# Performance work log

Hardware: AMD Instinct MI355X
Metric: run time of the kernel (lower is better)

## Reference

```python
import jax, jax.numpy as jnp
import numpy as np
import math

N_TOTAL = 262144
C = 128
B = 512
LMAX = 512  # max segment length (static for jit)


def setup_inputs() -> dict:
    key = jax.random.key(0)
    ks = jax.random.split(key, 8)
    Q_feature = jax.random.normal(ks[0], (N_TOTAL, C), dtype=jnp.float32)
    K_feature = jax.random.normal(ks[1], (N_TOTAL, C), dtype=jnp.float32)
    # cumulative offsets: equal segments of length LMAX (general code handles ragged)
    offset = (jnp.arange(1, B + 1, dtype=jnp.int64) * (N_TOTAL // B))
    s = 1.0 / math.sqrt(C)
    Wq = jax.random.normal(ks[2], (C, C), dtype=jnp.float32) * s
    Wk = jax.random.normal(ks[3], (C, C), dtype=jnp.float32) * s
    Wv = jax.random.normal(ks[4], (C, C), dtype=jnp.float32) * s
    bq = jnp.zeros((C,), dtype=jnp.float32)
    bk = jnp.zeros((C,), dtype=jnp.float32)
    bv = jnp.zeros((C,), dtype=jnp.float32)
    return {"Q_feature": Q_feature, "K_feature": K_feature,
            "Wq": Wq, "bq": bq, "Wk": Wk, "bk": bk, "Wv": Wv, "bv": bv,
            "offset": offset}


def reference(Q_feature, K_feature, Wq, bq, Wk, bk, Wv, bv, offset):
    N, Cdim = Q_feature.shape
    Q = Q_feature @ Wq.T + bq
    K = K_feature @ Wk.T + bk
    V = K_feature @ Wv.T + bv

    starts = jnp.concatenate([jnp.zeros((1,), offset.dtype), offset[:-1]])
    lengths = offset - starts                         # (B,)
    pos = jnp.arange(LMAX)                            # (LMAX,)
    idx = jnp.clip(starts[:, None] + pos[None, :], 0, N - 1)  # (B, LMAX)
    mask = pos[None, :] < lengths[:, None]            # (B, LMAX) valid tokens

    Qp = Q[idx]                                       # (B, LMAX, C)
    Kp = K[idx]
    Vp = V[idx]

    scale = 1.0 / math.sqrt(Cdim)
    scores = jnp.einsum('blc,bmc->blm', Qp, Kp) * scale     # (B, LMAX, LMAX)
    scores = jnp.where(mask[:, None, :], scores, jnp.float32(-1e30))
    attn = jax.nn.softmax(scores, axis=-1)
    outp = jnp.einsum('blm,bmc->blc', attn, Vp)             # (B, LMAX, C)
    outp = outp * mask[:, :, None]                          # zero padded rows

    # scatter padded segments back to flat (N, C); idx is an exact partition on valid rows
    out = jnp.zeros((N, Cdim), dtype=outp.dtype).at[idx].add(outp)
    return out
```

## Files before the change

kernel.cpp:

```cpp
#include <hip/hip_runtime.h>
#include <hip/hip_bf16.h>

#define CDIM 128
#define LMAXC 512
#define QBLK 128
#define KVBLK 64

#define QSCALE (0.08838834764831845f * 1.4426950408889634f)

typedef __attribute__((ext_vector_type(8))) short bf16x8;
typedef __attribute__((ext_vector_type(4))) short bf16x4;
typedef __attribute__((ext_vector_type(4))) float f32x4;

__device__ inline unsigned pk2(float lo, float hi) {
    unsigned r;
    asm("v_cvt_pk_bf16_f32 %0, %1, %2" : "=v"(r) : "v"(lo), "v"(hi));
    return r;
}

__device__ inline bf16x8 cvt8v(float4 a, float4 b) {
    union { bf16x8 v; unsigned u[4]; } t;
    t.u[0] = pk2(a.x, a.y); t.u[1] = pk2(a.z, a.w);
    t.u[2] = pk2(b.x, b.y); t.u[3] = pk2(b.z, b.w);
    return t.v;
}

__device__ inline void gload16(const void* g, void* l) {
    __builtin_amdgcn_global_load_lds(
        (const __attribute__((address_space(1))) unsigned*)g,
        (__attribute__((address_space(3))) unsigned*)l, 16, 0, 0);
}

__device__ inline void blk_barrier() {
    __builtin_amdgcn_sched_barrier(0);
    __builtin_amdgcn_s_barrier();
    __builtin_amdgcn_sched_barrier(0);
}

__device__ inline int pch(int q) { return ((q + (q >> 3)) & 7) << 4; }

__global__ void wcvt_kernel(const float* __restrict__ Wq,
                            const float* __restrict__ Wk,
                            const float* __restrict__ Wv,
                            short* __restrict__ Wbf)
{
    int t = blockIdx.x * 256 + threadIdx.x;
    int m = t / 2048;
    int e = (t % 2048) * 8;
    const float* W = (m == 0) ? Wq : (m == 1) ? Wk : Wv;
    float sc = (m == 0) ? QSCALE : 1.0f;
    float4 a = *reinterpret_cast<const float4*>(W + e);
    float4 b = *reinterpret_cast<const float4*>(W + e + 4);
    a.x *= sc; a.y *= sc; a.z *= sc; a.w *= sc;
    b.x *= sc; b.y *= sc; b.z *= sc; b.w *= sc;
    *reinterpret_cast<bf16x8*>(Wbf + m * 16384 + e) = cvt8v(a, b);
}

__global__ __launch_bounds__(256) void proj_kernel(
    const float* __restrict__ Qf, const float* __restrict__ Kf,
    const short* __restrict__ Wbf,
    const float* __restrict__ bq, const float* __restrict__ bk,
    const float* __restrict__ bv,
    short* __restrict__ Qp, short* __restrict__ Kp, short* __restrict__ Vt,
    int N)
{
    __shared__ __align__(16) char vt_lds[32768];

    const int tid   = threadIdx.x;
    const int lane  = tid & 63;
    const int wv    = tid >> 6;
    const int lrow  = lane & 15;
    const int lhalf = lane >> 4;
    const int row0  = blockIdx.x * 128;
    const bool isQ  = (blockIdx.y == 0);
    const float* X  = isQ ? Qf : Kf;

    bf16x8 xfr[2][4];
#pragma unroll
    for (int xt = 0; xt < 2; ++xt) {
        const float* xr = X + (size_t)(row0 + wv * 32 + xt * 16 + lrow) * CDIM;
#pragma unroll
        for (int ks = 0; ks < 4; ++ks) {
            const float4* s = reinterpret_cast<const float4*>(xr + ks * 32 + lhalf * 8);
            xfr[xt][ks] = cvt8v(s[0], s[1]);
        }
    }

    {
        const short* W    = isQ ? Wbf : Wbf + 16384;
        const float* bias = isQ ? bq : bk;
        const float  bsc  = isQ ? QSCALE : 1.0f;
        short* outp       = isQ ? Qp : Kp;

#pragma unroll
        for (int cf = 0; cf < 8; ++cf) {
            const short* wr = W + (cf * 16 + lrow) * CDIM;
            bf16x8 wfr[4];
#pragma unroll
            for (int ks = 0; ks < 4; ++ks)
                wfr[ks] = *reinterpret_cast<const bf16x8*>(wr + ks * 32 + lhalf * 8);
            float4 bv4 = *reinterpret_cast<const float4*>(bias + cf * 16 + lhalf * 4);
#pragma unroll
            for (int xt = 0; xt < 2; ++xt) {
                f32x4 acc = {0.f, 0.f, 0.f, 0.f};
#pragma unroll
                for (int ks = 0; ks < 4; ++ks)
                    acc = __builtin_amdgcn_mfma_f32_16x16x32_bf16(wfr[ks], xfr[xt][ks], acc, 0, 0, 0);
                union { bf16x4 v; unsigned u[2]; } pk;
                pk.u[0] = pk2(acc[0] + bv4.x * bsc, acc[1] + bv4.y * bsc);
                pk.u[1] = pk2(acc[2] + bv4.z * bsc, acc[3] + bv4.w * bsc);
                *reinterpret_cast<bf16x4*>(
                    outp + (size_t)(row0 + wv * 32 + xt * 16 + lrow) * CDIM
                         + cf * 16 + lhalf * 4) = pk.v;
            }
        }
    }

    if (!isQ) {
        const short* W = Wbf + 32768;
#pragma unroll
        for (int cf = 0; cf < 8; ++cf) {
            f32x4 acc0 = {0.f, 0.f, 0.f, 0.f};
            f32x4 acc1 = {0.f, 0.f, 0.f, 0.f};
            const short* wr = W + (cf * 16 + lrow) * CDIM;
#pragma unroll
            for (int ks = 0; ks < 4; ++ks) {
                bf16x8 bfr = *reinterpret_cast<const bf16x8*>(wr + ks * 32 + lhalf * 8);
                acc0 = __builtin_amdgcn_mfma_f32_16x16x32_bf16(xfr[0][ks], bfr, acc0, 0, 0, 0);
                acc1 = __builtin_amdgcn_mfma_f32_16x16x32_bf16(xfr[1][ks], bfr, acc1, 0, 0, 0);
            }
            const int col = cf * 16 + lrow;
            float bcol = bv[col];
            union { bf16x4 v; unsigned u[2]; } p0, p1;
            p0.u[0] = pk2(acc0[0] + bcol, acc0[1] + bcol);
            p0.u[1] = pk2(acc0[2] + bcol, acc0[3] + bcol);
            p1.u[0] = pk2(acc1[0] + bcol, acc1[1] + bcol);
            p1.u[1] = pk2(acc1[2] + bcol, acc1[3] + bcol);
            int base = col * 256 + wv * 64 + lhalf * 8;
            int sw   = (col & 7) << 4;
            *reinterpret_cast<bf16x4*>(vt_lds + ((base)      ^ sw)) = p0.v;
            *reinterpret_cast<bf16x4*>(vt_lds + ((base + 32) ^ sw)) = p1.v;
        }
        __syncthreads();
#pragma unroll
        for (int it = 0; it < 8; ++it) {
            int c   = it * 256 + tid;
            int col = c >> 4, rc = c & 15;
            int a   = (col * 256 + rc * 16) ^ ((col & 7) << 4);
            bf16x8 v = *reinterpret_cast<const bf16x8*>(vt_lds + a);
            *reinterpret_cast<bf16x8*>(Vt + (size_t)col * N + row0 + rc * 8) = v;
        }
    }
}

__global__ __launch_bounds__(256) void attn_kernel(
    const short* __restrict__ Qp, const short* __restrict__ Kp,
    const short* __restrict__ VtG, const int* __restrict__ offset,
    float* __restrict__ out, int Ntot)
{
    __shared__ __align__(16) char smem[81920];
    char* lds_p = smem + 65536;

    const int nq = LMAXC / QBLK;
    int flat = blockIdx.x, total = gridDim.x;
    int seg, qb;
    if ((total & (8 * nq - 1)) == 0) {
        int per = total >> 3;
        int xcd = flat & 7;
        int wi  = flat >> 3;
        int sl  = wi / nq;
        qb  = wi - sl * nq;
        seg = xcd * (per / nq) + sl;
    } else { seg = flat / nq; qb = flat - seg * nq; }

    const int start = (seg == 0) ? 0 : offset[seg - 1];
    int len = offset[seg] - start;
    if (len > LMAXC) len = LMAXC;
    const int q0 = qb * QBLK;
    if (q0 >= len) return;

    const int tid   = threadIdx.x;
    const int lane  = tid & 63;
    const int wv    = tid >> 6;
    const int lrow  = lane & 15;
    const int lhalf = lane >> 4;
    const int ntiles = (len + KVBLK - 1) / KVBLK;
    const int lm1 = len - 1;

    auto stage = [&](int kv0, int bb) {
        char* kb = smem + bb * 32768;
        char* vb = kb + 16384;
#pragma unroll
        for (int j = 0; j < 4; ++j) {
            int beta = j * 4096 + wv * 1024 + (lane << 4);
            int r  = beta >> 8;
            int gs = ((beta >> 4) & 15) ^ (r & 7);
            int rg = kv0 + r; if (rg > lm1) rg = lm1;
            gload16(Kp + (((size_t)(start + rg)) << 7) + (gs << 3),
                    kb + j * 4096 + wv * 1024);
            int d   = beta >> 7;
            int gs2 = ((beta >> 4) & 7) ^ (d & 7);
            long gk = (long)start + kv0 + (gs2 << 3);
            if (gk + 8 > Ntot) gk = Ntot - 8;
            gload16(VtG + (size_t)d * Ntot + gk,
                    vb + j * 4096 + wv * 1024);
        }
    };

    stage(0, 0);

    bf16x8 aq[2][4];
#pragma unroll
    for (int qt = 0; qt < 2; ++qt) {
        int qr = q0 + wv * 32 + qt * 16 + lrow;
        if (qr > lm1) qr = lm1;
        const short* qrow = Qp + (size_t)(start + qr) * CDIM;
#pragma unroll
        for (int ks = 0; ks < 4; ++ks)
            aq[qt][ks] = *reinterpret_cast<const bf16x8*>(qrow + ks * 32 + lhalf * 8);
    }

    f32x4 acc_o[2][8];
    float lsum[2] = {0.f, 0.f};
#pragma unroll
    for (int qt = 0; qt < 2; ++qt)
#pragma unroll
        for (int df = 0; df < 8; ++df) acc_o[qt][df] = (f32x4){0.f, 0.f, 0.f, 0.f};

    const int wbase = wv * 4096;

    for (int t = 0; t < ntiles; ++t) {
        const int kv0 = t * KVBLK;
        const int bb  = t & 1;
        if (t + 1 < ntiles) {
            stage(kv0 + KVBLK, bb ^ 1);
            asm volatile("s_waitcnt vmcnt(8)" ::: "memory");
        } else {
            asm volatile("s_waitcnt vmcnt(0)" ::: "memory");
        }
        blk_barrier();

        char* lds_k  = smem + bb * 32768;
        char* lds_vt = lds_k + 16384;
        const bool tail = (kv0 + KVBLK > len);

        f32x4 s0[4], s1[4];
        __builtin_amdgcn_s_setprio(1);
#pragma unroll
        for (int kf = 0; kf < 4; ++kf) {
            s0[kf] = (f32x4){0.f, 0.f, 0.f, 0.f};
            s1[kf] = (f32x4){0.f, 0.f, 0.f, 0.f};
            int key = kf * 16 + lrow;
#pragma unroll
            for (int ks = 0; ks < 4; ++ks) {
                int kbo = (key * 256 + (ks * 32 + lhalf * 8) * 2) ^ ((key & 7) << 4);
                bf16x8 kfr = *reinterpret_cast<const bf16x8*>(lds_k + kbo);
                s0[kf] = __builtin_amdgcn_mfma_f32_16x16x32_bf16(kfr, aq[0][ks], s0[kf], 0, 0, 0);
                s1[kf] = __builtin_amdgcn_mfma_f32_16x16x32_bf16(kfr, aq[1][ks], s1[kf], 0, 0, 0);
            }
        }
        __builtin_amdgcn_s_setprio(0);

        const int keyb0 = kv0 + lhalf * 4;
#pragma unroll
        for (int qt = 0; qt < 2; ++qt) {
            const int qlocal = qt * 16 + lrow;
            const int rowoff = wbase + qlocal * 128;
            const int swz = pch(qlocal);
#pragma unroll
            for (int kf = 0; kf < 4; ++kf) {
                f32x4 sv = qt ? s1[kf] : s0[kf];
                float p[4];
#pragma unroll
                for (int r = 0; r < 4; ++r) {
                    float pv = exp2f(sv[r]);
                    if (tail && (keyb0 + kf * 16 + r >= len)) pv = 0.f;
                    p[r] = pv;
                    lsum[qt] += pv;
                }
                unsigned long long w =
                    (unsigned long long)pk2(p[0], p[1]) |
                    ((unsigned long long)pk2(p[2], p[3]) << 32);
                *reinterpret_cast<unsigned long long*>(
                    lds_p + rowoff + ((kf * 32 + lhalf * 8) ^ swz)) = w;
            }
        }

        __builtin_amdgcn_s_setprio(1);
#pragma unroll
        for (int ks2 = 0; ks2 < 2; ++ks2) {
            bf16x8 ap0 = *reinterpret_cast<const bf16x8*>(
                lds_p + wbase + lrow * 128 + ((ks2 * 64 + lhalf * 16) ^ pch(lrow)));
            bf16x8 ap1 = *reinterpret_cast<const bf16x8*>(
                lds_p + wbase + (16 + lrow) * 128 + ((ks2 * 64 + lhalf * 16) ^ pch(16 + lrow)));
            int k0 = ks2 * 32 + lhalf * 8;
#pragma unroll
            for (int df = 0; df < 8; ++df) {
                int d = df * 16 + lrow;
                int vb2 = (d * 128 + k0 * 2) ^ ((d & 7) << 4);
                bf16x8 bvf = *reinterpret_cast<const bf16x8*>(lds_vt + vb2);
                acc_o[0][df] = __builtin_amdgcn_mfma_f32_16x16x32_bf16(ap0, bvf, acc_o[0][df], 0, 0, 0);
                acc_o[1][df] = __builtin_amdgcn_mfma_f32_16x16x32_bf16(ap1, bvf, acc_o[1][df], 0, 0, 0);
            }
        }
        __builtin_amdgcn_s_setprio(0);

        blk_barrier();
    }

#pragma unroll
    for (int qt = 0; qt < 2; ++qt) {
        float l = lsum[qt];
        l += __shfl_xor(l, 16);
        l += __shfl_xor(l, 32);
        float rinv[4];
#pragma unroll
        for (int r = 0; r < 4; ++r)
            rinv[r] = 1.0f / __shfl(l, lhalf * 4 + r);
#pragma unroll
        for (int df = 0; df < 8; ++df)
#pragma unroll
            for (int r = 0; r < 4; ++r) {
                int qg = q0 + wv * 32 + qt * 16 + lhalf * 4 + r;
                if (qg < len)
                    out[(size_t)(start + qg) * CDIM + df * 16 + lrow]
                        = acc_o[qt][df][r] * rinv[r];
            }
    }
}

extern "C" void kernel_launch(void* const* d_in, const int* in_sizes, int n_in,
                              void* d_out, int out_size, void* d_ws, size_t ws_size,
                              hipStream_t stream) {
    const float* Qf = (const float*)d_in[0];
    const float* Kf = (const float*)d_in[1];
    const float* Wq = (const float*)d_in[2];
    const float* bq = (const float*)d_in[3];
    const float* Wk = (const float*)d_in[4];
    const float* bk = (const float*)d_in[5];
    const float* Wv = (const float*)d_in[6];
    const float* bv_ = (const float*)d_in[7];
    const int* offset = (const int*)d_in[8];

    const int N = in_sizes[0] / CDIM;
    const int B = in_sizes[8];

    short* Qp = (short*)d_ws;
    short* Kp = Qp + (size_t)N * CDIM;
    short* Vt = Kp + (size_t)N * CDIM;
    float* out = (float*)d_out;

    size_t base_need = (size_t)3 * N * CDIM * 2;
    short* Wbf = (ws_size >= base_need + 3 * 16384 * 2)
               ? (Vt + (size_t)N * CDIM) : (short*)d_out;

    wcvt_kernel<<<24, 256, 0, stream>>>(Wq, Wk, Wv, Wbf);

    dim3 pgrid(N / 128, 2);
    proj_kernel<<<pgrid, 256, 0, stream>>>(Qf, Kf, Wbf, bq, bk, bv_,
                                           Qp, Kp, Vt, N);

    attn_kernel<<<dim3(B * (LMAXC / QBLK)), 256, 0, stream>>>(
        Qp, Kp, Vt, offset, out, N);
}
```

Baseline: 279.2 us.

## Halve projection LDS staging and raise occupancy target for proj_kernel

The V-transpose staging buffer in the projection kernel is cut to half size and processed in two phases of 64 columns, with an extra barrier between phases. The launch bounds now request 8 blocks per SM so more waves can be resident. The hardware packed bf16 conversion is also replaced by a software round-to-nearest-even routine. These changes trade extra barriers and more ALU work per conversion for lower LDS use and potentially higher occupancy in a memory-bound kernel.

```diff
diff --git a/kernel.cpp b/kernel.cpp
--- a/kernel.cpp
+++ b/kernel.cpp
@@ -12,17 +12,23 @@
 typedef __attribute__((ext_vector_type(4))) short bf16x4;
 typedef __attribute__((ext_vector_type(4))) float f32x4;
 
+__device__ inline short f2bf(float f) {
+    union { float f; unsigned u; } v; v.f = f;
+    unsigned r = v.u + 0x7FFFu + ((v.u >> 16) & 1u);
+    return (short)(r >> 16);
+}
+
+__device__ inline bf16x8 cvt8v(float4 a, float4 b) {
+    bf16x8 o;
+    o[0] = f2bf(a.x); o[1] = f2bf(a.y); o[2] = f2bf(a.z); o[3] = f2bf(a.w);
+    o[4] = f2bf(b.x); o[5] = f2bf(b.y); o[6] = f2bf(b.z); o[7] = f2bf(b.w);
+    return o;
+}
+
 __device__ inline unsigned pk2(float lo, float hi) {
     unsigned r;
     asm("v_cvt_pk_bf16_f32 %0, %1, %2" : "=v"(r) : "v"(lo), "v"(hi));
     return r;
-}
-
-__device__ inline bf16x8 cvt8v(float4 a, float4 b) {
-    union { bf16x8 v; unsigned u[4]; } t;
-    t.u[0] = pk2(a.x, a.y); t.u[1] = pk2(a.z, a.w);
-    t.u[2] = pk2(b.x, b.y); t.u[3] = pk2(b.z, b.w);
-    return t.v;
 }
 
 __device__ inline void gload16(const void* g, void* l) {
@@ -56,7 +62,7 @@
     *reinterpret_cast<bf16x8*>(Wbf + m * 16384 + e) = cvt8v(a, b);
 }
 
-__global__ __launch_bounds__(256) void proj_kernel(
+__global__ __launch_bounds__(256, 8) void proj_kernel(
     const float* __restrict__ Qf, const float* __restrict__ Kf,
     const short* __restrict__ Wbf,
     const float* __restrict__ bq, const float* __restrict__ bk,
@@ -64,7 +70,7 @@
     short* __restrict__ Qp, short* __restrict__ Kp, short* __restrict__ Vt,
     int N)
 {
-    __shared__ __align__(16) char vt_lds[32768];
+    __shared__ __align__(16) char vt_lds[16384];
 
     const int tid   = threadIdx.x;
     const int lane  = tid & 63;
@@ -106,12 +112,14 @@
 #pragma unroll
                 for (int ks = 0; ks < 4; ++ks)
                     acc = __builtin_amdgcn_mfma_f32_16x16x32_bf16(wfr[ks], xfr[xt][ks], acc, 0, 0, 0);
-                union { bf16x4 v; unsigned u[2]; } pk;
-                pk.u[0] = pk2(acc[0] + bv4.x * bsc, acc[1] + bv4.y * bsc);
-                pk.u[1] = pk2(acc[2] + bv4.z * bsc, acc[3] + bv4.w * bsc);
+                bf16x4 pk;
+                pk[0] = f2bf(acc[0] + bv4.x * bsc);
+                pk[1] = f2bf(acc[1] + bv4.y * bsc);
+                pk[2] = f2bf(acc[2] + bv4.z * bsc);
+                pk[3] = f2bf(acc[3] + bv4.w * bsc);
                 *reinterpret_cast<bf16x4*>(
                     outp + (size_t)(row0 + wv * 32 + xt * 16 + lrow) * CDIM
-                         + cf * 16 + lhalf * 4) = pk.v;
+                         + cf * 16 + lhalf * 4) = pk;
             }
         }
     }
@@ -119,36 +127,43 @@
     if (!isQ) {
         const short* W = Wbf + 32768;
 #pragma unroll
-        for (int cf = 0; cf < 8; ++cf) {
-            f32x4 acc0 = {0.f, 0.f, 0.f, 0.f};
-            f32x4 acc1 = {0.f, 0.f, 0.f, 0.f};
-            const short* wr = W + (cf * 16 + lrow) * CDIM;
-#pragma unroll
-            for (int ks = 0; ks < 4; ++ks) {
-                bf16x8 bfr = *reinterpret_cast<const bf16x8*>(wr + ks * 32 + lhalf * 8);
-                acc0 = __builtin_amdgcn_mfma_f32_16x16x32_bf16(xfr[0][ks], bfr, acc0, 0, 0, 0);
-                acc1 = __builtin_amdgcn_mfma_f32_16x16x32_bf16(xfr[1][ks], bfr, acc1, 0, 0, 0);
-            }
-            const int col = cf * 16 + lrow;
-            float bcol = bv[col];
-            union { bf16x4 v; unsigned u[2]; } p0, p1;
-            p0.u[0] = pk2(acc0[0] + bcol, acc0[1] + bcol);
-            p0.u[1] = pk2(acc0[2] + bcol, acc0[3] + bcol);
-            p1.u[0] = pk2(acc1[0] + bcol, acc1[1] + bcol);
-            p1.u[1] = pk2(acc1[2] + bcol, acc1[3] + bcol);
-            int base = col * 256 + wv * 64 + lhalf * 8;
-            int sw   = (col & 7) << 4;
-            *reinterpret_cast<bf16x4*>(vt_lds + ((base)      ^ sw)) = p0.v;
-            *reinterpret_cast<bf16x4*>(vt_lds + ((base + 32) ^ sw)) = p1.v;
-        }
-        __syncthreads();
-#pragma unroll
-        for (int it = 0; it < 8; ++it) {
-            int c   = it * 256 + tid;
-            int col = c >> 4, rc = c & 15;
-            int a   = (col * 256 + rc * 16) ^ ((col & 7) << 4);
-            bf16x8 v = *reinterpret_cast<const bf16x8*>(vt_lds + a);
-            *reinterpret_cast<bf16x8*>(Vt + (size_t)col * N + row0 + rc * 8) = v;
+        for (int ph = 0; ph < 2; ++ph) {
+#pragma unroll
+            for (int c4 = 0; c4 < 4; ++c4) {
+                const int cf = ph * 4 + c4;
+                f32x4 acc0 = {0.f, 0.f, 0.f, 0.f};
+                f32x4 acc1 = {0.f, 0.f, 0.f, 0.f};
+                const short* wr = W + (cf * 16 + lrow) * CDIM;
+#pragma unroll
+                for (int ks = 0; ks < 4; ++ks) {
+                    bf16x8 bfr = *reinterpret_cast<const bf16x8*>(wr + ks * 32 + lhalf * 8);
+                    acc0 = __builtin_amdgcn_mfma_f32_16x16x32_bf16(xfr[0][ks], bfr, acc0, 0, 0, 0);
+                    acc1 = __builtin_amdgcn_mfma_f32_16x16x32_bf16(xfr[1][ks], bfr, acc1, 0, 0, 0);
+                }
+                const int colL = c4 * 16 + lrow;
+                float bcol = bv[ph * 64 + colL];
+                bf16x4 p0, p1;
+#pragma unroll
+                for (int r = 0; r < 4; ++r) {
+                    p0[r] = f2bf(acc0[r] + bcol);
+                    p1[r] = f2bf(acc1[r] + bcol);
+                }
+                int base = colL * 256 + wv * 64 + lhalf * 8;
+                int sw   = (colL & 7) << 4;
+                *reinterpret_cast<bf16x4*>(vt_lds + ((base)      ^ sw)) = p0;
+                *reinterpret_cast<bf16x4*>(vt_lds + ((base + 32) ^ sw)) = p1;
+            }
+            __syncthreads();
+#pragma unroll
+            for (int it = 0; it < 4; ++it) {
+                int c    = it * 256 + tid;
+                int colL = c >> 4, rc = c & 15;
+                int a    = (colL * 256 + rc * 16) ^ ((colL & 7) << 4);
+                bf16x8 v = *reinterpret_cast<const bf16x8*>(vt_lds + a);
+                *reinterpret_cast<bf16x8*>(
+                    Vt + (size_t)(ph * 64 + colL) * N + row0 + rc * 8) = v;
+            }
+            __syncthreads();
         }
     }
 }
```

After: 469.3 us. 1.68x slower.
